# Performance work log

Measured on AMD Instinct MI355X. Metric: run time of the kernel, lower is better.

Reference implementation:

```python
import jax, jax.numpy as jnp
import numpy as np

N_EXPERTS = 256
N_GROUP = 8
TOPK_GROUP = 4
TOP_K = 8
NORM_TOPK_PROB = True
ROUTED_SCALING_FACTOR = 2.5
NUM_TOKENS = 262144


def setup_inputs() -> dict:
    key = jax.random.key(0)
    k1, k2 = jax.random.split(key)
    router_logits = jax.random.normal(k1, (NUM_TOKENS, N_EXPERTS), dtype=jnp.float32)
    e_score_correction_bias = jax.random.normal(k2, (N_EXPERTS,), dtype=jnp.float32) * 0.1
    return {"router_logits": router_logits, "e_score_correction_bias": e_score_correction_bias}


def reference(router_logits, e_score_correction_bias):
    experts_per_group = N_EXPERTS // N_GROUP  # 32
    scores = jax.nn.sigmoid(router_logits)                       # [T, E]
    scores_for_choice = scores + e_score_correction_bias          # [T, E]

    # group score = sum of top-2 expert scores within each group
    grouped = scores_for_choice.reshape(-1, N_GROUP, experts_per_group)  # [T, G, E/G]
    top2_vals, _ = jax.lax.top_k(grouped, 2)                      # [T, G, 2]
    group_scores = top2_vals.sum(axis=-1)                         # [T, G]

    # keep top `TOPK_GROUP` groups
    _, group_idx = jax.lax.top_k(group_scores, TOPK_GROUP)        # [T, topk_group]
    group_mask = jnp.sum(jax.nn.one_hot(group_idx, N_GROUP, dtype=jnp.bool_), axis=1)  # [T, G]
    score_mask = jnp.repeat(group_mask, experts_per_group, axis=-1)  # [T, E]

    masked_scores = jnp.where(score_mask, scores_for_choice, 0.0)
    _, topk_indices = jax.lax.top_k(masked_scores, TOP_K)         # [T, top_k]

    topk_weights = jnp.take_along_axis(scores, topk_indices, axis=-1)  # [T, top_k]
    if NORM_TOPK_PROB:
        denom = topk_weights.sum(axis=-1, keepdims=True) + 1e-20
        topk_weights = topk_weights / denom
    topk_weights = topk_weights * ROUTED_SCALING_FACTOR
    return topk_indices, topk_weights
```

## Files before the change

kernel.cpp:

```cpp
#include <hip/hip_runtime.h>
#include <stdint.h>

#define NE 256
#define TKG 4
#define TK 8
#define TPB 64
#define CDW 66
#define CNT_OFF 64

typedef float pf2 __attribute__((ext_vector_type(2)));

__device__ __forceinline__ pf2 pk_fma_ss(pf2 a, pf2 b, pf2 cs) {
    pf2 d; asm("v_pk_fma_f32 %0, %1, %2, %3" : "=v"(d) : "v"(a), "v"(b), "s"(cs)); return d;
}
__device__ __forceinline__ pf2 pk_fma_sv(pf2 as, pf2 b, pf2 c) {
    pf2 d; asm("v_pk_fma_f32 %0, %1, %2, %3" : "=v"(d) : "s"(as), "v"(b), "v"(c)); return d;
}
__device__ __forceinline__ pf2 pk_fma_vv(pf2 a, pf2 b, pf2 c) {
    pf2 d; asm("v_pk_fma_f32 %0, %1, %2, %3" : "=v"(d) : "v"(a), "v"(b), "v"(c)); return d;
}
__device__ __forceinline__ pf2 pk_mul_s(pf2 a, pf2 bs) {
    pf2 d; asm("v_pk_mul_f32 %0, %1, %2" : "=v"(d) : "v"(a), "s"(bs)); return d;
}
__device__ __forceinline__ pf2 pk_mul_v(pf2 a, pf2 b) {
    pf2 d; asm("v_pk_mul_f32 %0, %1, %2" : "=v"(d) : "v"(a), "v"(b)); return d;
}
__device__ __forceinline__ pf2 pk_add_s(pf2 a, pf2 bs) {
    pf2 d; asm("v_pk_add_f32 %0, %1, %2" : "=v"(d) : "v"(a), "s"(bs)); return d;
}
__device__ __forceinline__ pf2 pk_add_v(pf2 a, pf2 b) {
    pf2 d; asm("v_pk_add_f32 %0, %1, %2" : "=v"(d) : "v"(a), "v"(b)); return d;
}

__device__ __forceinline__ pf2 np_expf2(pf2 v, int* qi0, int* qi1) {
    const pf2 LOG2E  = {1.44269504088896341f, 1.44269504088896341f};
    const pf2 MAGIC  = {12582912.0f, 12582912.0f};
    const pf2 NMAGIC = {-12582912.0f, -12582912.0f};
    const pf2 NLN2HI = {-0.693359375f, -0.693359375f};
    const pf2 LN2LO  = {2.12194440e-4f, 2.12194440e-4f};
    const pf2 A0     = {1.9875691500E-4f, 1.9875691500E-4f};
    const pf2 A1     = {1.3981999507E-3f, 1.3981999507E-3f};
    const pf2 A2     = {8.3334519073E-3f, 8.3334519073E-3f};
    const pf2 A3     = {4.1665795894E-2f, 4.1665795894E-2f};
    const pf2 A4     = {1.6666665459E-1f, 1.6666665459E-1f};
    const pf2 A5     = {5.0000001201E-1f, 5.0000001201E-1f};
    const pf2 ONE    = {1.0f, 1.0f};

    pf2 m = pk_mul_s(v, LOG2E);
    pf2 y = pk_add_s(m, MAGIC);
    pf2 qf = pk_add_s(y, NMAGIC);
    *qi0 = __float_as_int(y.x) - 0x4B400000;
    *qi1 = __float_as_int(y.y) - 0x4B400000;
    pf2 t = pk_fma_sv(NLN2HI, qf, v);
    t = pk_fma_sv(LN2LO, qf, t);
    pf2 t2 = pk_mul_v(t, t);
    pf2 p = pk_fma_sv(A0, t, A1);
    p = pk_fma_ss(p, t, A2);
    p = pk_fma_ss(p, t, A3);
    p = pk_fma_ss(p, t, A4);
    p = pk_fma_ss(p, t, A5);
    p = pk_fma_vv(p, t2, t);
    p = pk_add_s(p, ONE);
    return p;
}

__device__ __forceinline__ pf2 crdiv2(pf2 d) {
    const pf2 NEG1 = {-1.0f, -1.0f};
    const pf2 ONE  = {1.0f, 1.0f};
    pf2 nd = pk_mul_s(d, NEG1);
    pf2 y0;
    y0.x = __builtin_amdgcn_rcpf(d.x);
    y0.y = __builtin_amdgcn_rcpf(d.y);
    pf2 e0 = pk_fma_ss(nd, y0, ONE);
    pf2 y1 = pk_fma_vv(e0, y0, y0);
    pf2 e1 = pk_fma_ss(nd, y1, ONE);
    pf2 y2 = pk_fma_vv(e1, y1, y1);
    pf2 r  = pk_fma_ss(nd, y2, ONE);
    return pk_fma_vv(r, y2, y2);
}

__device__ __forceinline__ unsigned ordkey(float v) {
    int b = __float_as_int(v);
    return (unsigned)(b ^ ((b >> 31) | 0x80000000));
}
__device__ __forceinline__ float inv_ordkey(unsigned u) {
    unsigned b = (u & 0x80000000u) ? (u ^ 0x80000000u) : ~u;
    return __uint_as_float(b);
}

__device__ __forceinline__ float rlanef(float v, int l) {
    return __int_as_float(__builtin_amdgcn_readlane(__float_as_int(v), l));
}
__device__ __forceinline__ unsigned rlaneu(unsigned v, int l) {
    return (unsigned)__builtin_amdgcn_readlane((int)v, l);
}
__device__ __forceinline__ unsigned umax_(unsigned a, unsigned b) { return a > b ? a : b; }
__device__ __forceinline__ int mbcnt64(unsigned long long m) {
    return __builtin_amdgcn_mbcnt_hi((unsigned)(m >> 32),
           __builtin_amdgcn_mbcnt_lo((unsigned)m, 0u));
}

template <int CTRL>
__device__ __forceinline__ float dppf(float x) {
    int xi = __float_as_int(x);
    return __int_as_float(__builtin_amdgcn_update_dpp(xi, xi, CTRL, 0xF, 0xF, false));
}
#define DPP_XOR1  0xB1
#define DPP_XOR2  0x4E
#define DPP_HMIRR 0x141
#define DPP_ROR8  0x128
#define DPP_BC15  0x142
#define DPP_BC31  0x143

#define INS8(cand) do {                                                \
    const uint64_t c_ = (cand);                                        \
    const bool q0 = c_ > v0, q1 = c_ > v1, q2 = c_ > v2, q3 = c_ > v3; \
    const bool q4 = c_ > v4, q5 = c_ > v5, q6 = c_ > v6, q7 = c_ > v7; \
    v7 = q7 ? (q6 ? v6 : c_) : v7;                                     \
    v6 = q6 ? (q5 ? v5 : c_) : v6;                                     \
    v5 = q5 ? (q4 ? v4 : c_) : v5;                                     \
    v4 = q4 ? (q3 ? v3 : c_) : v4;                                     \
    v3 = q3 ? (q2 ? v2 : c_) : v3;                                     \
    v2 = q2 ? (q1 ? v1 : c_) : v2;                                     \
    v1 = q1 ? (q0 ? v0 : c_) : v1;                                     \
    v0 = q0 ? c_ : v0;                                                 \
} while (0)

__device__ __forceinline__ void score_token(
    const float4 cur, const pf2 biasL, const pf2 biasH,
    const int lane, const int bpa, uint32_t* row)
{
    const pf2 ONE = {1.0f, 1.0f};
    int qa0, qa1, qb0, qb1;
    pf2 pA = np_expf2((pf2){-cur.x, -cur.y}, &qa0, &qa1);
    pf2 pB = np_expf2((pf2){-cur.z, -cur.w}, &qb0, &qb1);
    pf2 eA, eB;
    eA.x = ldexpf(pA.x, qa0);
    eA.y = ldexpf(pA.y, qa1);
    eB.x = ldexpf(pB.x, qb0);
    eB.y = ldexpf(pB.y, qb1);
    pf2 dA = pk_add_s(eA, ONE);
    pf2 dB = pk_add_s(eB, ONE);
    pf2 sA = crdiv2(dA);
    pf2 sB = crdiv2(dB);
    pf2 cA = pk_add_v(sA, biasL);
    pf2 cB = pk_add_v(sB, biasH);
    const float c0 = cA.x, c1 = cA.y, c2 = cB.x, c3 = cB.y;

    float a1 = fmaxf(c0, c1), a2 = fminf(c0, c1);
    float d1 = fmaxf(c2, c3), d2 = fminf(c2, c3);
    float m1 = fmaxf(a1, d1);
    float m2 = fmaxf(fminf(a1, d1), fmaxf(a2, d2));

    {
        float p1 = dppf<DPP_XOR1>(m1), p2 = dppf<DPP_XOR1>(m2);
        float n1 = fmaxf(m1, p1);
        m2 = fmaxf(fminf(m1, p1), fmaxf(m2, p2)); m1 = n1;
    }
    {
        float p1 = dppf<DPP_XOR2>(m1), p2 = dppf<DPP_XOR2>(m2);
        float n1 = fmaxf(m1, p1);
        m2 = fmaxf(fminf(m1, p1), fmaxf(m2, p2)); m1 = n1;
    }
    {
        float p1 = dppf<DPP_HMIRR>(m1), p2 = dppf<DPP_HMIRR>(m2);
        float n1 = fmaxf(m1, p1);
        m2 = fmaxf(fminf(m1, p1), fmaxf(m2, p2)); m1 = n1;
    }
    const float gs = m1 + m2;

    const float gb = __int_as_float(
        __builtin_amdgcn_ds_bpermute(bpa, __float_as_int(gs)));
    const unsigned long long gtm = __ballot(gb > gs);
    const unsigned long long eqm = __ballot(gb == gs);
    const unsigned long long term = gtm | (eqm & 0x7F3F1F0F07030100ull);
    unsigned km8 = 0;
    #pragma unroll
    for (int a = 0; a < 8; ++a)
        km8 |= (unsigned)(__popcll((term >> (8 * a)) & 0xFFull) < 4 ? 1u : 0u) << a;
    const int g = lane >> 3;
    const bool keep = (km8 >> g) & 1u;

    const float inf_ = __uint_as_float(0x7F800000u);
    float mm = keep ? m2 : inf_;
    mm = fminf(mm, dppf<DPP_ROR8>(mm));
    mm = fminf(mm, dppf<DPP_BC15>(mm));
    mm = fminf(mm, dppf<DPP_BC31>(mm));
    const float t0f = rlanef(mm, 63);

    const bool cd0 = keep && (c0 >= t0f);
    const bool cd1 = keep && (c1 >= t0f);
    const bool cd2 = keep && (c2 >= t0f);
    const bool cd3 = keep && (c3 >= t0f);
    const unsigned long long b0 = __ballot(cd0);
    const unsigned long long b1 = __ballot(cd1);
    const unsigned long long b2 = __ballot(cd2);
    const unsigned long long b3 = __ballot(cd3);
    const unsigned p1_ = __popcll(b0);
    const unsigned p2_ = p1_ + __popcll(b1);
    const unsigned p3_ = p2_ + __popcll(b2);
    unsigned cnt = p3_ + __popcll(b3);

    const unsigned k0 = ordkey(c0);
    const unsigned k1 = ordkey(c1);
    const unsigned k2 = ordkey(c2);
    const unsigned k3 = ordkey(c3);

    const int base = lane * 4;
    if (cnt <= 32u) {
        if (cd0) *reinterpret_cast<uint64_t*>(&row[2 * (0u  + mbcnt64(b0))]) =
            ((uint64_t)k0 << 32) | (unsigned)(255 - base);
        if (cd1) *reinterpret_cast<uint64_t*>(&row[2 * (p1_ + mbcnt64(b1))]) =
            ((uint64_t)k1 << 32) | (unsigned)(255 - base - 1);
        if (cd2) *reinterpret_cast<uint64_t*>(&row[2 * (p2_ + mbcnt64(b2))]) =
            ((uint64_t)k2 << 32) | (unsigned)(255 - base - 2);
        if (cd3) *reinterpret_cast<uint64_t*>(&row[2 * (p3_ + mbcnt64(b3))]) =
            ((uint64_t)k3 << 32) | (unsigned)(255 - base - 3);
    } else {
        unsigned mk0 = keep ? k0 : 0x80000000u;
        unsigned mk1 = keep ? k1 : 0x80000000u;
        unsigned mk2 = keep ? k2 : 0x80000000u;
        unsigned mk3 = keep ? k3 : 0x80000000u;
        for (int r = 0; r < TK; ++r) {
            unsigned h = umax_(umax_(mk0, mk1), umax_(mk2, mk3));
            unsigned m = h;
            m = umax_(m, (unsigned)__shfl_xor((int)m, 1));
            m = umax_(m, (unsigned)__shfl_xor((int)m, 2));
            m = umax_(m, (unsigned)__shfl_xor((int)m, 4));
            m = umax_(m, (unsigned)__shfl_xor((int)m, 8));
            const unsigned M = umax_(umax_(rlaneu(m, 0), rlaneu(m, 16)),
                                     umax_(rlaneu(m, 32), rlaneu(m, 48)));
            const unsigned long long bl = __ballot(h == M);
            const int wl = __ffsll(bl) - 1;
            const unsigned long long sb0 = __ballot(mk0 == M);
            const unsigned long long sb1 = __ballot(mk1 == M);
            const unsigned long long sb2 = __ballot(mk2 == M);
            const int slot = ((sb0 >> wl) & 1) ? 0 : ((sb1 >> wl) & 1) ? 1
                           : ((sb2 >> wl) & 1) ? 2 : 3;
            if (lane == r)
                *reinterpret_cast<uint64_t*>(&row[2 * r]) =
                    ((uint64_t)M << 32) | (unsigned)(255 - (wl * 4 + slot));
            const bool iw = (lane == wl);
            mk0 = (iw && slot == 0) ? 0u : mk0;
            mk1 = (iw && slot == 1) ? 0u : mk1;
            mk2 = (iw && slot == 2) ? 0u : mk2;
            mk3 = (iw && slot == 3) ? 0u : mk3;
        }
        cnt = 8;
    }
    if (lane == 0) row[CNT_OFF] = cnt;
}

__global__ __launch_bounds__(256, 4) void route_kernel(
    const float* __restrict__ logits,
    const float* __restrict__ bias,
    float* __restrict__ out_idx_f,
    float* __restrict__ out_w,
    int T)
{
    __shared__ uint32_t cand[TPB * CDW];
    __shared__ float    bias_s[NE];

    const int lane = threadIdx.x & 63;
    const int wvi  = threadIdx.x >> 6;
    const long long tok0 = (long long)blockIdx.x * TPB;

    bias_s[threadIdx.x] = bias[threadIdx.x];

    {
        const float4 bias4 = *reinterpret_cast<const float4*>(bias + lane * 4);
        const pf2 biasL = {bias4.x, bias4.y};
        const pf2 biasH = {bias4.z, bias4.w};
        const float* lp = logits + (tok0 + wvi * 16) * NE + lane * 4;
        uint32_t* wrow = &cand[(wvi * 16) * CDW];
        const int bpa = (lane & 7) << 5;

        float4 cA = *reinterpret_cast<const float4*>(lp);
        float4 cB = *reinterpret_cast<const float4*>(lp + NE);
        float4 nA, nB;
        for (int i = 0; i < 8; ++i) {
            if (i < 7) {
                nA = *reinterpret_cast<const float4*>(lp + (2 * i + 2) * NE);
                nB = *reinterpret_cast<const float4*>(lp + (2 * i + 3) * NE);
            }
            score_token(cA, biasL, biasH, lane, bpa, wrow + (2 * i) * CDW);
            score_token(cB, biasL, biasH, lane, bpa, wrow + (2 * i + 1) * CDW);
            cA = nA; cB = nB;
        }
    }
    __syncthreads();

    if (threadIdx.x < TPB) {
        uint32_t* row = &cand[threadIdx.x * CDW];
        const long long t = tok0 + threadIdx.x;
        const unsigned cnt = row[CNT_OFF];

        uint64_t v0 = 0, v1 = 0, v2 = 0, v3 = 0, v4 = 0, v5 = 0, v6 = 0, v7 = 0;
        for (unsigned j = 0; j < cnt; ++j) {
            const uint64_t e = *reinterpret_cast<const uint64_t*>(&row[2 * j]);
            INS8(e);
        }

        const int e0 = 255 - (int)(v0 & 255u);
        const int e1 = 255 - (int)(v1 & 255u);
        const int e2 = 255 - (int)(v2 & 255u);
        const int e3 = 255 - (int)(v3 & 255u);
        const int e4 = 255 - (int)(v4 & 255u);
        const int e5 = 255 - (int)(v5 & 255u);
        const int e6 = 255 - (int)(v6 & 255u);
        const int e7 = 255 - (int)(v7 & 255u);
        const float s0 = inv_ordkey((unsigned)(v0 >> 32)) - bias_s[e0];
        const float s1 = inv_ordkey((unsigned)(v1 >> 32)) - bias_s[e1];
        const float s2 = inv_ordkey((unsigned)(v2 >> 32)) - bias_s[e2];
        const float s3 = inv_ordkey((unsigned)(v3 >> 32)) - bias_s[e3];
        const float s4 = inv_ordkey((unsigned)(v4 >> 32)) - bias_s[e4];
        const float s5 = inv_ordkey((unsigned)(v5 >> 32)) - bias_s[e5];
        const float s6 = inv_ordkey((unsigned)(v6 >> 32)) - bias_s[e6];
        const float s7 = inv_ordkey((unsigned)(v7 >> 32)) - bias_s[e7];

        const float denom = ((s0 + s1) + (s2 + s3)) + ((s4 + s5) + (s6 + s7));
        const float scale = 2.5f * __builtin_amdgcn_rcpf(denom + 1e-20f);

        float4* oi = reinterpret_cast<float4*>(out_idx_f + t * TK);
        float4* ow = reinterpret_cast<float4*>(out_w + t * TK);
        oi[0] = make_float4((float)e0, (float)e1, (float)e2, (float)e3);
        oi[1] = make_float4((float)e4, (float)e5, (float)e6, (float)e7);
        ow[0] = make_float4(s0 * scale, s1 * scale, s2 * scale, s3 * scale);
        ow[1] = make_float4(s4 * scale, s5 * scale, s6 * scale, s7 * scale);
    }
}

extern "C" void kernel_launch(void* const* d_in, const int* in_sizes, int n_in,
                              void* d_out, int out_size, void* d_ws, size_t ws_size,
                              hipStream_t stream) {
    const float* logits = (const float*)d_in[0];
    const float* bias   = (const float*)d_in[1];
    const int T = in_sizes[0] / NE;

    float* out_idx_f = (float*)d_out;
    float* out_w     = (float*)d_out + (size_t)T * TK;

    const int grid = T / TPB;
    route_kernel<<<grid, 256, 0, stream>>>(logits, bias, out_idx_f, out_w, T);
}
```

Baseline: 91.84 us.

## Branchless candidate stores, zero-padded rows, and 4-wide unrolled final insertion loop

Candidate writes become unconditional: lanes whose values do not qualify store to a per-lane trash slot, so the four guarded LDS stores turn into straight-line code. Each row is padded with zero entries after the count so the final top-8 insertion loop can read 128-bit pairs and process four candidates per iteration. The row stride grows to fit the padding, and the launch bound is raised to 5 blocks per CU for occupancy. In exchange the code does extra LDS writes and needs more shared memory per block, and the higher occupancy target may force register spills.

```diff
diff --git a/kernel.cpp b/kernel.cpp
--- a/kernel.cpp
+++ b/kernel.cpp
@@ -5,8 +5,8 @@
 #define TKG 4
 #define TK 8
 #define TPB 64
-#define CDW 66
-#define CNT_OFF 64
+#define CDW 76
+#define CNT_OFF 72
 
 typedef float pf2 __attribute__((ext_vector_type(2)));
 
@@ -128,7 +128,7 @@
 
 __device__ __forceinline__ void score_token(
     const float4 cur, const pf2 biasL, const pf2 biasH,
-    const int lane, const int bpa, uint32_t* row)
+    const int lane, const int bpa, uint32_t* row, uint32_t* trash)
 {
     const pf2 ONE = {1.0f, 1.0f};
     int qa0, qa1, qb0, qb1;
@@ -208,14 +208,15 @@
 
     const int base = lane * 4;
     if (cnt <= 32u) {
-        if (cd0) *reinterpret_cast<uint64_t*>(&row[2 * (0u  + mbcnt64(b0))]) =
-            ((uint64_t)k0 << 32) | (unsigned)(255 - base);
-        if (cd1) *reinterpret_cast<uint64_t*>(&row[2 * (p1_ + mbcnt64(b1))]) =
-            ((uint64_t)k1 << 32) | (unsigned)(255 - base - 1);
-        if (cd2) *reinterpret_cast<uint64_t*>(&row[2 * (p2_ + mbcnt64(b2))]) =
-            ((uint64_t)k2 << 32) | (unsigned)(255 - base - 2);
-        if (cd3) *reinterpret_cast<uint64_t*>(&row[2 * (p3_ + mbcnt64(b3))]) =
-            ((uint64_t)k3 << 32) | (unsigned)(255 - base - 3);
+        uint32_t* tr = &trash[lane * 2];
+        uint32_t* w0 = cd0 ? &row[2 * (0u  + mbcnt64(b0))] : tr;
+        uint32_t* w1 = cd1 ? &row[2 * (p1_ + mbcnt64(b1))] : tr;
+        uint32_t* w2 = cd2 ? &row[2 * (p2_ + mbcnt64(b2))] : tr;
+        uint32_t* w3 = cd3 ? &row[2 * (p3_ + mbcnt64(b3))] : tr;
+        *reinterpret_cast<uint64_t*>(w0) = ((uint64_t)k0 << 32) | (unsigned)(255 - base);
+        *reinterpret_cast<uint64_t*>(w1) = ((uint64_t)k1 << 32) | (unsigned)(255 - base - 1);
+        *reinterpret_cast<uint64_t*>(w2) = ((uint64_t)k2 << 32) | (unsigned)(255 - base - 2);
+        *reinterpret_cast<uint64_t*>(w3) = ((uint64_t)k3 << 32) | (unsigned)(255 - base - 3);
     } else {
         unsigned mk0 = keep ? k0 : 0x80000000u;
         unsigned mk1 = keep ? k1 : 0x80000000u;
@@ -248,10 +249,12 @@
         }
         cnt = 8;
     }
+    if (lane < 4)
+        *reinterpret_cast<uint64_t*>(&row[2 * (cnt + lane)]) = 0ull;
     if (lane == 0) row[CNT_OFF] = cnt;
 }
 
-__global__ __launch_bounds__(256, 4) void route_kernel(
+__global__ __launch_bounds__(256, 5) void route_kernel(
     const float* __restrict__ logits,
     const float* __restrict__ bias,
     float* __restrict__ out_idx_f,
@@ -259,6 +262,7 @@
     int T)
 {
     __shared__ uint32_t cand[TPB * CDW];
+    __shared__ uint32_t trash[128];
     __shared__ float    bias_s[NE];
 
     const int lane = threadIdx.x & 63;
@@ -283,8 +287,8 @@
                 nA = *reinterpret_cast<const float4*>(lp + (2 * i + 2) * NE);
                 nB = *reinterpret_cast<const float4*>(lp + (2 * i + 3) * NE);
             }
-            score_token(cA, biasL, biasH, lane, bpa, wrow + (2 * i) * CDW);
-            score_token(cB, biasL, biasH, lane, bpa, wrow + (2 * i + 1) * CDW);
+            score_token(cA, biasL, biasH, lane, bpa, wrow + (2 * i) * CDW, trash);
+            score_token(cB, biasL, biasH, lane, bpa, wrow + (2 * i + 1) * CDW, trash);
             cA = nA; cB = nB;
         }
     }
@@ -294,11 +298,14 @@
         uint32_t* row = &cand[threadIdx.x * CDW];
         const long long t = tok0 + threadIdx.x;
         const unsigned cnt = row[CNT_OFF];
+        const unsigned iters = (cnt + 3) >> 2;
 
         uint64_t v0 = 0, v1 = 0, v2 = 0, v3 = 0, v4 = 0, v5 = 0, v6 = 0, v7 = 0;
-        for (unsigned j = 0; j < cnt; ++j) {
-            const uint64_t e = *reinterpret_cast<const uint64_t*>(&row[2 * j]);
-            INS8(e);
+        const ulonglong2* rp = reinterpret_cast<const ulonglong2*>(row);
+        for (unsigned it = 0; it < iters; ++it) {
+            const ulonglong2 a = rp[2 * it];
+            const ulonglong2 b = rp[2 * it + 1];
+            INS8(a.x); INS8(a.y); INS8(b.x); INS8(b.y);
         }
 
         const int e0 = 255 - (int)(v0 & 255u);
```

New measurement: 93.65 us. About the same (+2.0%).
